# Kernel tuning notes

Hardware: AMD Instinct MI355X
Metric: run time of the kernel (lower is better)

Reference implementation:

```python
import jax, jax.numpy as jnp
import numpy as np

RANK = 16
BN_EPS = 1e-5


def _head(xf, qw, qb, kw, kb, vw, vb, qlw, klw, ow, ob):
    # xf: [B, S, c]  (c = split channels)
    Q = xf @ qw.T + qb
    K = xf @ kw.T + kb
    V = xf @ vw.T + vb
    Ql = Q @ qlw.T                      # [B, S, rank]
    Kl = K @ klw.T                      # [B, S, rank]
    scores = jnp.einsum('bsr,btr->bst', Ql, Kl) / jnp.sqrt(jnp.float32(RANK))
    attn = jax.nn.softmax(scores, axis=-1)   # [B, S, S]
    out = jnp.einsum('bst,btc->bsc', attn, V)
    return out @ ow.T + ob


def _bn(x, g, b):
    # training-mode BatchNorm2d: biased batch stats over (B, H, W)
    m = x.mean(axis=(0, 2, 3), keepdims=True)
    v = x.var(axis=(0, 2, 3), keepdims=True)
    return (x - m) / jnp.sqrt(v + BN_EPS) * g[None, :, None, None] + b[None, :, None, None]


def reference(x, qw, qb, kw, kb, vw, vb, qlw, klw, ow, ob,
              f1w, f1b, f2w, f2b, g1, b1, g2, b2):
    B, C, H, W = x.shape
    sc = C // 4
    S = H * W
    xf = x.reshape(B, C, S).transpose(0, 2, 1)   # [B, S, C]

    outs = []
    prev = jnp.zeros_like(xf[..., :sc])
    for i in range(4):  # hierarchical: head i consumes split_i + out_{i-1}
        xi = xf[..., i * sc:(i + 1) * sc] + prev
        prev = _head(xi, qw[i], qb[i], kw[i], kb[i], vw[i], vb[i],
                     qlw[i], klw[i], ow[i], ob[i])
        outs.append(prev)

    concat = jnp.concatenate(outs, axis=-1).transpose(0, 2, 1).reshape(B, C, H, W)
    out = x + _bn(concat, g1, b1)

    # FFN: 1x1 conv 256->1024, exact GELU, 1x1 conv 1024->256 (dropout = eval / identity)
    h = jnp.einsum('bchw,oc->bohw', out, f1w) + f1b[None, :, None, None]
    h = jax.nn.gelu(h, approximate=False)
    h = jnp.einsum('bchw,oc->bohw', h, f2w) + f2b[None, :, None, None]
    return out + _bn(h, g2, b2)


def setup_inputs() -> dict:
    key = jax.random.key(0)
    ks = jax.random.split(key, 16)
    B, C, H, W = 2, 256, 64, 64
    sc = C // 4
    s = 0.05
    inp = {
        'x':   jax.random.normal(ks[0], (B, C, H, W), jnp.float32),
        'qw':  jax.random.normal(ks[1], (4, sc, sc), jnp.float32) * s,
        'qb':  jnp.zeros((4, sc), jnp.float32),
        'kw':  jax.random.normal(ks[2], (4, sc, sc), jnp.float32) * s,
        'kb':  jnp.zeros((4, sc), jnp.float32),
        'vw':  jax.random.normal(ks[3], (4, sc, sc), jnp.float32) * s,
        'vb':  jnp.zeros((4, sc), jnp.float32),
        'qlw': jax.random.normal(ks[4], (4, RANK, sc), jnp.float32) * s,
        'klw': jax.random.normal(ks[5], (4, RANK, sc), jnp.float32) * s,
        'ow':  jax.random.normal(ks[6], (4, sc, sc), jnp.float32) * s,
        'ob':  jnp.zeros((4, sc), jnp.float32),
        'f1w': jax.random.normal(ks[7], (4 * C, C), jnp.float32) * s,
        'f1b': jnp.zeros((4 * C,), jnp.float32),
        'f2w': jax.random.normal(ks[8], (C, 4 * C), jnp.float32) * s,
        'f2b': jnp.zeros((C,), jnp.float32),
        'g1':  jnp.ones((C,), jnp.float32),
        'b1':  jnp.zeros((C,), jnp.float32),
        'g2':  jnp.ones((C,), jnp.float32),
        'b2':  jnp.zeros((C,), jnp.float32),
    }
    return inp
```

## Files before the change

### kernel.cpp

```cpp
#include <hip/hip_runtime.h>
#include <math.h>

#define SS 4096
#define CC 256
#define NB 2
#define KSPLIT 8
#define KCHUNK (SS / KSPLIT)
#define KT 64
#define QTM 128

typedef __bf16 bf16x8 __attribute__((ext_vector_type(8)));
typedef float f32x4 __attribute__((ext_vector_type(4)));

__device__ inline float b2f(unsigned short u) {
    union { float f; unsigned int i; } x; x.i = ((unsigned int)u) << 16; return x.f;
}

__global__ void prep_weights_kernel(const float* __restrict__ qw, const float* __restrict__ qb,
                                    const float* __restrict__ kw, const float* __restrict__ kb,
                                    const float* __restrict__ qlw, const float* __restrict__ klw,
                                    float* __restrict__ wq, float* __restrict__ wk,
                                    float* __restrict__ bq, float* __restrict__ bk)
{
    int i = blockIdx.x;
    int t = threadIdx.x;
    for (int idx = t; idx < 16 * 64; idx += 256) {
        int r = idx >> 6, c = idx & 63;
        float sq = 0.f, sk = 0.f;
        for (int j = 0; j < 64; ++j) {
            sq += qlw[(i * 16 + r) * 64 + j] * qw[(i * 64 + j) * 64 + c];
            sk += klw[(i * 16 + r) * 64 + j] * kw[(i * 64 + j) * 64 + c];
        }
        wq[i * 1024 + idx] = sq;
        wk[i * 1024 + idx] = sk;
    }
    if (t < 16) {
        float sq = 0.f, sk = 0.f;
        for (int j = 0; j < 64; ++j) {
            sq += qlw[(i * 16 + t) * 64 + j] * qb[i * 64 + j];
            sk += klw[(i * 16 + t) * 64 + j] * kb[i * 64 + j];
        }
        bq[i * 16 + t] = sq;
        bk[i * 16 + t] = sk;
    }
}

__global__ void transpose_x_kernel(const float* __restrict__ x, float* __restrict__ xT)
{
    __shared__ float tile[32][33];
    int b = blockIdx.z;
    int s0 = blockIdx.x * 32, c0 = blockIdx.y * 32;
    int tx = threadIdx.x, ty = threadIdx.y;
    const float* xb = x + (size_t)b * CC * SS;
    for (int j = 0; j < 4; ++j)
        tile[ty + 8 * j][tx] = xb[(size_t)(c0 + ty + 8 * j) * SS + s0 + tx];
    __syncthreads();
    float* xTb = xT + (size_t)b * SS * CC;
    for (int j = 0; j < 4; ++j)
        xTb[(size_t)(s0 + ty + 8 * j) * CC + c0 + tx] = tile[tx][ty + 8 * j];
}

__global__ void f32_to_bf16_kernel(const float* __restrict__ src, __bf16* __restrict__ dst, int n)
{
    int i = (blockIdx.x * 256 + threadIdx.x) * 4;
    if (i < n) {
        float4 v = *(const float4*)&src[i];
        union { uint2 u; __bf16 b[4]; } pk;
        pk.b[0] = (__bf16)v.x; pk.b[1] = (__bf16)v.y;
        pk.b[2] = (__bf16)v.z; pk.b[3] = (__bf16)v.w;
        *(uint2*)&dst[i] = pk.u;
    }
}

__global__ __launch_bounds__(256) void head_qkv_kernel(
    const float* __restrict__ xT, const float* __restrict__ conc,
    const float* __restrict__ wq, const float* __restrict__ wk,
    const float* __restrict__ bq, const float* __restrict__ bk,
    const float* __restrict__ vw, const float* __restrict__ vb,
    __bf16* __restrict__ Qlb, __bf16* __restrict__ Klb, __bf16* __restrict__ Vtb, int head)
{
    __shared__ float swq[16 * 65];
    __shared__ float swk[16 * 65];
    __shared__ float swv[64 * 65];
    __shared__ float sxi[16][65];
    __shared__ float sv16[64][17];
    __shared__ float sbq[16], sbk[16], sbv[64];

    int t = threadIdx.x;
    int b = blockIdx.y;
    int s0 = blockIdx.x * 16;

    for (int idx = t; idx < 16 * 64; idx += 256) {
        int r = idx >> 6, c = idx & 63;
        swq[r * 65 + c] = wq[head * 1024 + idx];
        swk[r * 65 + c] = wk[head * 1024 + idx];
    }
    for (int idx = t; idx < 64 * 64; idx += 256) {
        int r = idx >> 6, c = idx & 63;
        swv[r * 65 + c] = vw[head * 4096 + idx];
    }
    if (t < 16) { sbq[t] = bq[head * 16 + t]; sbk[t] = bk[head * 16 + t]; }
    if (t < 64) sbv[t] = vb[head * 64 + t];

    for (int idx = t; idx < 1024; idx += 256) {
        int r = idx >> 6, c = idx & 63;
        size_t row = (size_t)(b * SS + s0 + r);
        float v = xT[row * CC + head * 64 + c];
        if (head > 0) v += conc[row * CC + (head - 1) * 64 + c];
        sxi[r][c] = v;
    }
    __syncthreads();

    for (int idx = t; idx < 1536; idx += 256) {
        int r = idx / 96, o = idx % 96;
        const float* w;
        float acc;
        int kind;
        if (o < 16)      { w = &swq[o * 65];        acc = sbq[o];      kind = 0; }
        else if (o < 32) { w = &swk[(o - 16) * 65]; acc = sbk[o - 16]; kind = 1; }
        else             { w = &swv[(o - 32) * 65]; acc = sbv[o - 32]; kind = 2; }
        float s = 0.f;
        #pragma unroll 16
        for (int c = 0; c < 64; ++c) s += sxi[r][c] * w[c];
        acc += s;
        size_t row = (size_t)(b * SS + s0 + r);
        if (kind == 0)      Qlb[row * 16 + o] = (__bf16)(acc * 0.25f);
        else if (kind == 1) Klb[row * 16 + (o - 16)] = (__bf16)acc;
        else                sv16[o - 32][r] = acc;
    }
    __syncthreads();

    {
        int c = t >> 2, sq = t & 3;
        union { uint2 u; __bf16 bb[4]; } pk;
        #pragma unroll
        for (int j = 0; j < 4; ++j) pk.bb[j] = (__bf16)sv16[c][sq * 4 + j];
        *(uint2*)&Vtb[((size_t)b * 64 + c) * SS + s0 + sq * 4] = pk.u;
    }
}

__global__ __launch_bounds__(512) void attn_mfma_kernel(
    const __bf16* __restrict__ Qlb, const __bf16* __restrict__ Klb,
    const __bf16* __restrict__ Vtb,
    __bf16* __restrict__ pacc, float* __restrict__ pm, float* __restrict__ pl)
{
    __shared__ __align__(16) __bf16 sK[64 * 24];
    __shared__ __align__(16) __bf16 sVt[64 * 64];
    __shared__ __align__(16) __bf16 sP[8][16 * 64];

    const int t = threadIdx.x;
    const int lane = t & 63, wv = t >> 6;
    const int b = blockIdx.z, chunk = blockIdx.y;
    const int g = lane >> 4, qi = lane & 15;
    const int qrow = blockIdx.x * QTM + wv * 16 + qi;

    bf16x8 bQ;
    #pragma unroll
    for (int j = 0; j < 8; ++j) bQ[j] = (__bf16)0.f;
    if (lane < 32) bQ = *(const bf16x8*)(Qlb + ((size_t)b * SS + qrow) * 16 + g * 8);

    f32x4 acc[4];
    #pragma unroll
    for (int cs = 0; cs < 4; ++cs)
        #pragma unroll
        for (int r = 0; r < 4; ++r) acc[cs][r] = 0.f;
    float mrun = -1e30f, lrun = 0.f;

    __bf16* Pw = &sP[wv][0];
    const size_t kbase = (size_t)b * SS;
    const int kbeg = chunk * KCHUNK;

    for (int kt0 = kbeg; kt0 < kbeg + KCHUNK; kt0 += KT) {
        __syncthreads();
        if (t < 256) {
            int kk = t >> 2, quad = t & 3;
            *(uint2*)((char*)sK + kk * 48 + quad * 8) =
                *(const uint2*)(Klb + (kbase + kt0 + kk) * 16 + quad * 4);
        }
        {
            int c = t >> 3, sl = t & 7;
            int ksrc = (sl ^ (c & 7)) * 8;
            uint4 v = *(const uint4*)(Vtb + ((size_t)b * 64 + c) * SS + kt0 + ksrc);
            *(uint4*)((char*)sVt + c * 128 + sl * 16) = v;
        }
        __syncthreads();

        f32x4 st[4];
        #pragma unroll
        for (int ks = 0; ks < 4; ++ks) {
            bf16x8 aK;
            #pragma unroll
            for (int j = 0; j < 8; ++j) aK[j] = (__bf16)0.f;
            if (lane < 32)
                aK = *(const bf16x8*)((char*)sK + (ks * 16 + qi) * 48 + g * 16);
            f32x4 z;
            #pragma unroll
            for (int r = 0; r < 4; ++r) z[r] = 0.f;
            st[ks] = __builtin_amdgcn_mfma_f32_16x16x32_bf16(aK, bQ, z, 0, 0, 0);
        }

        float tmax = -1e30f;
        #pragma unroll
        for (int ks = 0; ks < 4; ++ks)
            #pragma unroll
            for (int r = 0; r < 4; ++r) tmax = fmaxf(tmax, st[ks][r]);
        tmax = fmaxf(tmax, __shfl_xor(tmax, 16));
        tmax = fmaxf(tmax, __shfl_xor(tmax, 32));
        float mnew = fmaxf(mrun, tmax);
        float scale = __expf(mrun - mnew);
        float psum = 0.f;
        #pragma unroll
        for (int ks = 0; ks < 4; ++ks) {
            union { uint2 u; __bf16 bb[4]; } pk;
            #pragma unroll
            for (int r = 0; r < 4; ++r) {
                float p = __expf(st[ks][r] - mnew);
                psum += p;
                pk.bb[r] = (__bf16)p;
            }
            int off = (qi * 128 + ks * 32 + g * 8) ^ ((qi & 7) << 4);
            *(uint2*)((char*)Pw + off) = pk.u;
        }
        psum += __shfl_xor(psum, 16);
        psum += __shfl_xor(psum, 32);
        lrun = lrun * scale + psum;
        mrun = mnew;
        #pragma unroll
        for (int cs = 0; cs < 4; ++cs) acc[cs] *= scale;

        #pragma unroll
        for (int kc = 0; kc < 2; ++kc) {
            int boff = (qi * 128 + kc * 64 + g * 16) ^ ((qi & 7) << 4);
            bf16x8 bP = *(const bf16x8*)((char*)Pw + boff);
            #pragma unroll
            for (int cs = 0; cs < 4; ++cs) {
                int c = cs * 16 + qi;
                int aoff = (c * 128 + kc * 64 + g * 16) ^ ((c & 7) << 4);
                bf16x8 aV = *(const bf16x8*)((char*)sVt + aoff);
                acc[cs] = __builtin_amdgcn_mfma_f32_16x16x32_bf16(aV, bP, acc[cs], 0, 0, 0);
            }
        }
    }

    size_t prow = (size_t)(b * KSPLIT + chunk) * SS + qrow;
    #pragma unroll
    for (int cs = 0; cs < 4; ++cs) {
        union { uint2 u; __bf16 bb[4]; } pk;
        #pragma unroll
        for (int r = 0; r < 4; ++r) pk.bb[r] = (__bf16)acc[cs][r];
        *(uint2*)(pacc + prow * 64 + cs * 16 + g * 4) = pk.u;
    }
    if (lane < 16) { pm[prow] = mrun; pl[prow] = lrun; }
}

__global__ __launch_bounds__(512) void attn_combine_kernel(
    const __bf16* __restrict__ pacc, const float* __restrict__ pm, const float* __restrict__ pl,
    const float* __restrict__ ow, const float* __restrict__ ob,
    float* __restrict__ conc, int head)
{
    __shared__ float sO[32][66];
    __shared__ float sOWt[64][68];
    __shared__ float sob[64];

    const int t = threadIdx.x;
    const int b = blockIdx.y;
    const int s0 = blockIdx.x * 32;
    const int q = t >> 4;
    const int gk = t & 15;
    const int vc0 = gk * 4;

    for (int idx = t; idx < 4096; idx += 512) {
        int co = idx >> 6, k = idx & 63;
        sOWt[k][co] = ow[head * 4096 + idx];
    }
    if (t < 64) sob[t] = ob[head * 64 + t];

    float pmv[KSPLIT];
    float mstar = -1e30f;
    #pragma unroll
    for (int c = 0; c < KSPLIT; ++c) {
        pmv[c] = pm[(size_t)(b * KSPLIT + c) * SS + s0 + q];
        mstar = fmaxf(mstar, pmv[c]);
    }
    float l = 0.f;
    float o0 = 0.f, o1 = 0.f, o2 = 0.f, o3 = 0.f;
    const unsigned short* pu = (const unsigned short*)pacc;
    #pragma unroll
    for (int c = 0; c < KSPLIT; ++c) {
        size_t prow = (size_t)(b * KSPLIT + c) * SS + s0 + q;
        float w = __expf(pmv[c] - mstar);
        l += w * pl[prow];
        ushort4 a4 = *(const ushort4*)&pu[prow * 64 + vc0];
        o0 += w * b2f(a4.x); o1 += w * b2f(a4.y); o2 += w * b2f(a4.z); o3 += w * b2f(a4.w);
    }
    float inv_l = 1.f / l;
    sO[q][vc0 + 0] = o0 * inv_l;
    sO[q][vc0 + 1] = o1 * inv_l;
    sO[q][vc0 + 2] = o2 * inv_l;
    sO[q][vc0 + 3] = o3 * inv_l;
    __syncthreads();

    float e0 = sob[vc0 + 0], e1 = sob[vc0 + 1], e2 = sob[vc0 + 2], e3 = sob[vc0 + 3];
    #pragma unroll 8
    for (int k = 0; k < 64; ++k) {
        float ov = sO[q][k];
        float4 w4 = *(const float4*)&sOWt[k][vc0];
        e0 += ov * w4.x; e1 += ov * w4.y; e2 += ov * w4.z; e3 += ov * w4.w;
    }
    float* cp = conc + (size_t)(b * SS + s0 + q) * CC + head * 64 + vc0;
    float4 r; r.x = e0; r.y = e1; r.z = e2; r.w = e3;
    *(float4*)cp = r;
}

__global__ void bn_stats_kernel(const float* __restrict__ data, float* __restrict__ sum,
                                float* __restrict__ sumsq, int rows_per_block)
{
    int t = threadIdx.x;
    int r0 = blockIdx.x * rows_per_block;
    float s = 0.f, ss = 0.f;
    for (int r = 0; r < rows_per_block; ++r) {
        float v = data[(size_t)(r0 + r) * CC + t];
        s += v; ss += v * v;
    }
    atomicAdd(&sum[t], s);
    atomicAdd(&sumsq[t], ss);
}

__global__ void bn_apply1_kernel(const float* __restrict__ xT, const float* __restrict__ conc,
                                 const float* __restrict__ sum, const float* __restrict__ sumsq,
                                 const float* __restrict__ g, const float* __restrict__ bta,
                                 float* __restrict__ out1, __bf16* __restrict__ out1b)
{
    size_t idx = (size_t)blockIdx.x * 256 + threadIdx.x;
    int c = threadIdx.x;
    float mean = sum[c] * (1.f / 8192.f);
    float var = sumsq[c] * (1.f / 8192.f) - mean * mean;
    float rstd = rsqrtf(var + 1e-5f);
    float v = xT[idx] + (conc[idx] - mean) * rstd * g[c] + bta[c];
    out1[idx] = v;
    out1b[idx] = (__bf16)v;
}

template<int MREP>
__global__ __launch_bounds__(256) void gemm_mfma_kernel(
    const __bf16* __restrict__ A, const __bf16* __restrict__ W,
    const float* __restrict__ bias, void* __restrict__ out,
    int N, int K, int mode)
{
    constexpr int BM = 2 * MREP * 16;
    __shared__ __align__(16) __bf16 sA[BM * 72];
    __shared__ __align__(16) __bf16 sB[64 * 72];

    const int t = threadIdx.x;
    const int lane = t & 63, wv = t >> 6;
    const int wm = wv & 1, wn = wv >> 1;
    const int g = lane >> 4, c = lane & 15;
    const int m0 = blockIdx.x * BM, n0 = blockIdx.y * 64;

    f32x4 acc[MREP][2];
    #pragma unroll
    for (int mi = 0; mi < MREP; ++mi)
        #pragma unroll
        for (int ni = 0; ni < 2; ++ni)
            #pragma unroll
            for (int r = 0; r < 4; ++r) acc[mi][ni][r] = 0.f;

    const int rS = t >> 3, ksS = (t & 7) * 8;

    for (int k0 = 0; k0 < K; k0 += 64) {
        __syncthreads();
        #pragma unroll
        for (int i = 0; i < MREP; ++i) {
            int r = rS + i * 32;
            *(uint4*)&sA[r * 72 + ksS] = *(const uint4*)&A[(size_t)(m0 + r) * K + k0 + ksS];
        }
        #pragma unroll
        for (int i = 0; i < 2; ++i) {
            int r = rS + i * 32;
            *(uint4*)&sB[r * 72 + ksS] = *(const uint4*)&W[(size_t)(n0 + r) * K + k0 + ksS];
        }
        __syncthreads();

        #pragma unroll
        for (int kk = 0; kk < 2; ++kk) {
            bf16x8 bfr[2];
            #pragma unroll
            for (int ni = 0; ni < 2; ++ni)
                bfr[ni] = *(const bf16x8*)&sB[(wn * 32 + ni * 16 + c) * 72 + kk * 32 + g * 8];
            #pragma unroll
            for (int mi = 0; mi < MREP; ++mi) {
                bf16x8 afr = *(const bf16x8*)&sA[(wm * MREP * 16 + mi * 16 + c) * 72 + kk * 32 + g * 8];
                #pragma unroll
                for (int ni = 0; ni < 2; ++ni)
                    acc[mi][ni] = __builtin_amdgcn_mfma_f32_16x16x32_bf16(afr, bfr[ni], acc[mi][ni], 0, 0, 0);
            }
        }
    }

    #pragma unroll
    for (int ni = 0; ni < 2; ++ni) {
        int col = n0 + wn * 32 + ni * 16 + c;
        float bb = bias[col];
        #pragma unroll
        for (int mi = 0; mi < MREP; ++mi) {
            int row0 = m0 + wm * MREP * 16 + mi * 16 + g * 4;
            #pragma unroll
            for (int r = 0; r < 4; ++r) {
                float v = acc[mi][ni][r] + bb;
                if (mode) {
                    v = 0.5f * v * (1.f + erff(v * 0.70710678118654752f));
                    ((__bf16*)out)[(size_t)(row0 + r) * N + col] = (__bf16)v;
                } else {
                    ((float*)out)[(size_t)(row0 + r) * N + col] = v;
                }
            }
        }
    }
}

__global__ void bn_final_kernel(const float* __restrict__ out1, const float* __restrict__ h2,
                                const float* __restrict__ sum, const float* __restrict__ sumsq,
                                const float* __restrict__ g, const float* __restrict__ bta,
                                float* __restrict__ out)
{
    __shared__ float tile[32][33];
    int b = blockIdx.z;
    int s0 = blockIdx.x * 32, c0 = blockIdx.y * 32;
    int tx = threadIdx.x, ty = threadIdx.y;
    for (int j = 0; j < 4; ++j) {
        int c = c0 + tx;
        int s = s0 + ty + 8 * j;
        size_t idx = ((size_t)b * SS + s) * CC + c;
        float mean = sum[c] * (1.f / 8192.f);
        float var = sumsq[c] * (1.f / 8192.f) - mean * mean;
        float rstd = rsqrtf(var + 1e-5f);
        tile[ty + 8 * j][tx] = out1[idx] + (h2[idx] - mean) * rstd * g[c] + bta[c];
    }
    __syncthreads();
    for (int j = 0; j < 4; ++j) {
        int c = c0 + ty + 8 * j;
        int s = s0 + tx;
        out[((size_t)b * CC + c) * SS + s] = tile[tx][ty + 8 * j];
    }
}

extern "C" void kernel_launch(void* const* d_in, const int* in_sizes, int n_in,
                              void* d_out, int out_size, void* d_ws, size_t ws_size,
                              hipStream_t stream)
{
    const float* x   = (const float*)d_in[0];
    const float* qw  = (const float*)d_in[1];
    const float* qb  = (const float*)d_in[2];
    const float* kw  = (const float*)d_in[3];
    const float* kb  = (const float*)d_in[4];
    const float* vw  = (const float*)d_in[5];
    const float* vb  = (const float*)d_in[6];
    const float* qlw = (const float*)d_in[7];
    const float* klw = (const float*)d_in[8];
    const float* ow  = (const float*)d_in[9];
    const float* ob  = (const float*)d_in[10];
    const float* f1w = (const float*)d_in[11];
    const float* f1b = (const float*)d_in[12];
    const float* f2w = (const float*)d_in[13];
    const float* f2b = (const float*)d_in[14];
    const float* g1  = (const float*)d_in[15];
    const float* b1  = (const float*)d_in[16];
    const float* g2  = (const float*)d_in[17];
    const float* b2  = (const float*)d_in[18];
    float* outp = (float*)d_out;

    float* ws = (float*)d_ws;
    size_t off = 0;
    float* xT    = ws + off; off += (size_t)NB * SS * CC;
    float* conc  = ws + off; off += (size_t)NB * SS * CC;
    float* out1  = ws + off; off += (size_t)NB * SS * CC;
    float* h2    = ws + off; off += (size_t)NB * SS * CC;
    float* Hreg  = ws + off; off += (size_t)NB * SS * 1024 / 2;
    __bf16* out1b = (__bf16*)(ws + off); off += (size_t)NB * SS * CC / 2;
    __bf16* Qlb  = (__bf16*)(ws + off); off += (size_t)NB * SS * 16 / 2;
    __bf16* Klb  = (__bf16*)(ws + off); off += (size_t)NB * SS * 16 / 2;
    __bf16* Vtb  = (__bf16*)(ws + off); off += (size_t)NB * 64 * SS / 2;
    __bf16* f1wb = (__bf16*)(ws + off); off += (size_t)1024 * CC / 2;
    __bf16* f2wb = (__bf16*)(ws + off); off += (size_t)CC * 1024 / 2;
    float* wq_e  = ws + off; off += 4 * 1024;
    float* wk_e  = ws + off; off += 4 * 1024;
    float* bq_e  = ws + off; off += 64;
    float* bk_e  = ws + off; off += 64;
    float* stats = ws + off; off += 1024;
    float* sum1 = stats, *sumsq1 = stats + 256, *sum2 = stats + 512, *sumsq2 = stats + 768;

    __bf16* pacc = (__bf16*)Hreg;
    float* pm = Hreg + (size_t)NB * KSPLIT * SS * 64 / 2;
    float* pl = pm + (size_t)NB * KSPLIT * SS;
    __bf16* h1b = (__bf16*)Hreg;

    hipMemsetAsync(stats, 0, 1024 * sizeof(float), stream);

    prep_weights_kernel<<<4, 256, 0, stream>>>(qw, qb, kw, kb, qlw, klw, wq_e, wk_e, bq_e, bk_e);
    transpose_x_kernel<<<dim3(SS / 32, CC / 32, NB), dim3(32, 8), 0, stream>>>(x, xT);
    f32_to_bf16_kernel<<<(1024 * CC) / 1024, 256, 0, stream>>>(f1w, f1wb, 1024 * CC);
    f32_to_bf16_kernel<<<(CC * 1024) / 1024, 256, 0, stream>>>(f2w, f2wb, CC * 1024);

    for (int head = 0; head < 4; ++head) {
        head_qkv_kernel<<<dim3(SS / 16, NB), 256, 0, stream>>>(
            xT, conc, wq_e, wk_e, bq_e, bk_e, vw, vb, Qlb, Klb, Vtb, head);
        attn_mfma_kernel<<<dim3(SS / QTM, KSPLIT, NB), 512, 0, stream>>>(
            Qlb, Klb, Vtb, pacc, pm, pl);
        attn_combine_kernel<<<dim3(SS / 32, NB), 512, 0, stream>>>(
            pacc, pm, pl, ow, ob, conc, head);
    }

    bn_stats_kernel<<<128, 256, 0, stream>>>(conc, sum1, sumsq1, (NB * SS) / 128);
    bn_apply1_kernel<<<(NB * SS * CC) / 256, 256, 0, stream>>>(
        xT, conc, sum1, sumsq1, g1, b1, out1, out1b);

    gemm_mfma_kernel<4><<<dim3((NB * SS) / 128, 1024 / 64), 256, 0, stream>>>(
        out1b, f1wb, f1b, (void*)h1b, 1024, CC, 1);
    gemm_mfma_kernel<2><<<dim3((NB * SS) / 64, CC / 64), 256, 0, stream>>>(
        h1b, f2wb, f2b, (void*)h2, CC, 1024, 0);

    bn_stats_kernel<<<128, 256, 0, stream>>>(h2, sum2, sumsq2, (NB * SS) / 128);
    bn_final_kernel<<<dim3(SS / 32, CC / 32, NB), dim3(32, 8), 0, stream>>>(
        out1, h2, sum2, sumsq2, g2, b2, outp);
}
```

Before: 362.7 us.

## Use MFMA for head QKV projection, fuse BN stats into producers, store bf16 intermediates

The per-head QKV projection now runs on MFMA with bf16 weights prepacked into one buffer, and each block covers 32 rows instead of 16. BatchNorm statistics are accumulated inside the attention-combine kernel and the second FFN GEMM through shared and global atomics, so both standalone bn_stats passes are gone. The out1 and h2 intermediates are stored only in bf16, which cuts memory traffic but lowers the precision of the residual path and the final output.

```diff
diff --git a/kernel.cpp b/kernel.cpp
--- a/kernel.cpp
+++ b/kernel.cpp
@@ -18,9 +18,9 @@
 
 __global__ void prep_weights_kernel(const float* __restrict__ qw, const float* __restrict__ qb,
                                     const float* __restrict__ kw, const float* __restrict__ kb,
+                                    const float* __restrict__ vw, const float* __restrict__ vb,
                                     const float* __restrict__ qlw, const float* __restrict__ klw,
-                                    float* __restrict__ wq, float* __restrict__ wk,
-                                    float* __restrict__ bq, float* __restrict__ bk)
+                                    __bf16* __restrict__ Wall, float* __restrict__ bias_all)
 {
     int i = blockIdx.x;
     int t = threadIdx.x;
@@ -31,18 +31,21 @@
             sq += qlw[(i * 16 + r) * 64 + j] * qw[(i * 64 + j) * 64 + c];
             sk += klw[(i * 16 + r) * 64 + j] * kw[(i * 64 + j) * 64 + c];
         }
-        wq[i * 1024 + idx] = sq;
-        wk[i * 1024 + idx] = sk;
-    }
+        Wall[i * 6144 + idx] = (__bf16)(0.25f * sq);
+        Wall[i * 6144 + 1024 + idx] = (__bf16)sk;
+    }
+    for (int idx = t; idx < 64 * 64; idx += 256)
+        Wall[i * 6144 + 2048 + idx] = (__bf16)vw[i * 4096 + idx];
     if (t < 16) {
         float sq = 0.f, sk = 0.f;
         for (int j = 0; j < 64; ++j) {
             sq += qlw[(i * 16 + t) * 64 + j] * qb[i * 64 + j];
             sk += klw[(i * 16 + t) * 64 + j] * kb[i * 64 + j];
         }
-        bq[i * 16 + t] = sq;
-        bk[i * 16 + t] = sk;
-    }
+        bias_all[i * 96 + t] = 0.25f * sq;
+        bias_all[i * 96 + 16 + t] = sk;
+    }
+    if (t < 64) bias_all[i * 96 + 32 + t] = vb[i * 64 + t];
 }
 
 __global__ void transpose_x_kernel(const float* __restrict__ x, float* __restrict__ xT)
@@ -72,70 +75,80 @@
     }
 }
 
-__global__ __launch_bounds__(256) void head_qkv_kernel(
+__global__ __launch_bounds__(256) void head_qkv_mfma_kernel(
     const float* __restrict__ xT, const float* __restrict__ conc,
-    const float* __restrict__ wq, const float* __restrict__ wk,
-    const float* __restrict__ bq, const float* __restrict__ bk,
-    const float* __restrict__ vw, const float* __restrict__ vb,
+    const __bf16* __restrict__ Wall, const float* __restrict__ bias_all,
     __bf16* __restrict__ Qlb, __bf16* __restrict__ Klb, __bf16* __restrict__ Vtb, int head)
 {
-    __shared__ float swq[16 * 65];
-    __shared__ float swk[16 * 65];
-    __shared__ float swv[64 * 65];
-    __shared__ float sxi[16][65];
-    __shared__ float sv16[64][17];
-    __shared__ float sbq[16], sbk[16], sbv[64];
-
-    int t = threadIdx.x;
-    int b = blockIdx.y;
-    int s0 = blockIdx.x * 16;
-
-    for (int idx = t; idx < 16 * 64; idx += 256) {
-        int r = idx >> 6, c = idx & 63;
-        swq[r * 65 + c] = wq[head * 1024 + idx];
-        swk[r * 65 + c] = wk[head * 1024 + idx];
-    }
-    for (int idx = t; idx < 64 * 64; idx += 256) {
-        int r = idx >> 6, c = idx & 63;
-        swv[r * 65 + c] = vw[head * 4096 + idx];
-    }
-    if (t < 16) { sbq[t] = bq[head * 16 + t]; sbk[t] = bk[head * 16 + t]; }
-    if (t < 64) sbv[t] = vb[head * 64 + t];
-
-    for (int idx = t; idx < 1024; idx += 256) {
-        int r = idx >> 6, c = idx & 63;
-        size_t row = (size_t)(b * SS + s0 + r);
-        float v = xT[row * CC + head * 64 + c];
-        if (head > 0) v += conc[row * CC + (head - 1) * 64 + c];
-        sxi[r][c] = v;
+    __shared__ __align__(16) __bf16 sXi[32 * 72];
+    __shared__ __align__(16) __bf16 sW[96 * 72];
+    __shared__ __align__(16) __bf16 sVtT[64 * 40];
+    __shared__ float sBias[96];
+
+    const int t = threadIdx.x;
+    const int b = blockIdx.y;
+    const int s0 = blockIdx.x * 32;
+    const int lane = t & 63, wv = t >> 6;
+    const int wm = wv & 1, wnh = wv >> 1;
+    const int c = lane & 15, g = lane >> 4;
+
+    #pragma unroll
+    for (int i = 0; i < 6; ++i) {
+        int e = t + i * 256;
+        int row = e >> 4, c4 = (e & 15) * 4;
+        *(uint2*)&sW[row * 72 + c4] = *(const uint2*)&Wall[head * 6144 + row * 64 + c4];
+    }
+    if (t < 96) sBias[t] = bias_all[head * 96 + t];
+
+    #pragma unroll
+    for (int i = 0; i < 2; ++i) {
+        int idx = t + i * 256;
+        int row = idx >> 4, c4 = (idx & 15) * 4;
+        size_t grow = (size_t)(b * SS + s0 + row);
+        float4 v = *(const float4*)&xT[grow * CC + head * 64 + c4];
+        if (head > 0) {
+            float4 p = *(const float4*)&conc[grow * CC + (head - 1) * 64 + c4];
+            v.x += p.x; v.y += p.y; v.z += p.z; v.w += p.w;
+        }
+        union { uint2 u; __bf16 bb[4]; } pk;
+        pk.bb[0] = (__bf16)v.x; pk.bb[1] = (__bf16)v.y;
+        pk.bb[2] = (__bf16)v.z; pk.bb[3] = (__bf16)v.w;
+        *(uint2*)&sXi[row * 72 + c4] = pk.u;
     }
     __syncthreads();
 
-    for (int idx = t; idx < 1536; idx += 256) {
-        int r = idx / 96, o = idx % 96;
-        const float* w;
-        float acc;
-        int kind;
-        if (o < 16)      { w = &swq[o * 65];        acc = sbq[o];      kind = 0; }
-        else if (o < 32) { w = &swk[(o - 16) * 65]; acc = sbk[o - 16]; kind = 1; }
-        else             { w = &swv[(o - 32) * 65]; acc = sbv[o - 32]; kind = 2; }
-        float s = 0.f;
-        #pragma unroll 16
-        for (int c = 0; c < 64; ++c) s += sxi[r][c] * w[c];
-        acc += s;
-        size_t row = (size_t)(b * SS + s0 + r);
-        if (kind == 0)      Qlb[row * 16 + o] = (__bf16)(acc * 0.25f);
-        else if (kind == 1) Klb[row * 16 + (o - 16)] = (__bf16)acc;
-        else                sv16[o - 32][r] = acc;
+    bf16x8 aX0 = *(const bf16x8*)&sXi[(wm * 16 + c) * 72 + g * 8];
+    bf16x8 aX1 = *(const bf16x8*)&sXi[(wm * 16 + c) * 72 + 32 + g * 8];
+
+    #pragma unroll
+    for (int nt = 0; nt < 3; ++nt) {
+        int ntile = wnh * 3 + nt;
+        bf16x8 bW0 = *(const bf16x8*)&sW[(ntile * 16 + c) * 72 + g * 8];
+        bf16x8 bW1 = *(const bf16x8*)&sW[(ntile * 16 + c) * 72 + 32 + g * 8];
+        f32x4 d;
+        #pragma unroll
+        for (int r = 0; r < 4; ++r) d[r] = 0.f;
+        d = __builtin_amdgcn_mfma_f32_16x16x32_bf16(aX0, bW0, d, 0, 0, 0);
+        d = __builtin_amdgcn_mfma_f32_16x16x32_bf16(aX1, bW1, d, 0, 0, 0);
+
+        int ch = ntile * 16 + c;
+        float bb = sBias[ch];
+        int srow_l0 = wm * 16 + g * 4;
+        #pragma unroll
+        for (int r = 0; r < 4; ++r) {
+            float v = d[r] + bb;
+            int srow = s0 + srow_l0 + r;
+            if (ntile == 0)      Qlb[((size_t)b * SS + srow) * 16 + ch] = (__bf16)v;
+            else if (ntile == 1) Klb[((size_t)b * SS + srow) * 16 + (ch - 16)] = (__bf16)v;
+            else                 sVtT[(ch - 32) * 40 + srow_l0 + r] = (__bf16)v;
+        }
     }
     __syncthreads();
 
     {
-        int c = t >> 2, sq = t & 3;
-        union { uint2 u; __bf16 bb[4]; } pk;
-        #pragma unroll
-        for (int j = 0; j < 4; ++j) pk.bb[j] = (__bf16)sv16[c][sq * 4 + j];
-        *(uint2*)&Vtb[((size_t)b * 64 + c) * SS + s0 + sq * 4] = pk.u;
+        int ch = t >> 2, chunk = t & 3;
+        *(uint4*)&Vtb[((size_t)b * 64 + ch) * SS + s0 + chunk * 8] =
+            *(const uint4*)&sVtT[ch * 40 + chunk * 8];
     }
 }
 
@@ -256,11 +269,12 @@
 __global__ __launch_bounds__(512) void attn_combine_kernel(
     const __bf16* __restrict__ pacc, const float* __restrict__ pm, const float* __restrict__ pl,
     const float* __restrict__ ow, const float* __restrict__ ob,
-    float* __restrict__ conc, int head)
+    float* __restrict__ conc, float* __restrict__ gsum, float* __restrict__ gss, int head)
 {
     __shared__ float sO[32][66];
     __shared__ float sOWt[64][68];
     __shared__ float sob[64];
+    __shared__ float lsum[64], lss[64];
 
     const int t = threadIdx.x;
     const int b = blockIdx.y;
@@ -269,6 +283,7 @@
     const int gk = t & 15;
     const int vc0 = gk * 4;
 
+    if (t < 64) { lsum[t] = 0.f; lss[t] = 0.f; }
     for (int idx = t; idx < 4096; idx += 512) {
         int co = idx >> 6, k = idx & 63;
         sOWt[k][co] = ow[head * 4096 + idx];
@@ -300,36 +315,45 @@
     sO[q][vc0 + 3] = o3 * inv_l;
     __syncthreads();
 
-    float e0 = sob[vc0 + 0], e1 = sob[vc0 + 1], e2 = sob[vc0 + 2], e3 = sob[vc0 + 3];
+    float e[4];
+    #pragma unroll
+    for (int j = 0; j < 4; ++j) e[j] = sob[vc0 + j];
     #pragma unroll 8
     for (int k = 0; k < 64; ++k) {
         float ov = sO[q][k];
         float4 w4 = *(const float4*)&sOWt[k][vc0];
-        e0 += ov * w4.x; e1 += ov * w4.y; e2 += ov * w4.z; e3 += ov * w4.w;
+        e[0] += ov * w4.x; e[1] += ov * w4.y; e[2] += ov * w4.z; e[3] += ov * w4.w;
     }
     float* cp = conc + (size_t)(b * SS + s0 + q) * CC + head * 64 + vc0;
-    float4 r; r.x = e0; r.y = e1; r.z = e2; r.w = e3;
+    float4 r; r.x = e[0]; r.y = e[1]; r.z = e[2]; r.w = e[3];
     *(float4*)cp = r;
-}
-
-__global__ void bn_stats_kernel(const float* __restrict__ data, float* __restrict__ sum,
-                                float* __restrict__ sumsq, int rows_per_block)
-{
-    int t = threadIdx.x;
-    int r0 = blockIdx.x * rows_per_block;
-    float s = 0.f, ss = 0.f;
-    for (int r = 0; r < rows_per_block; ++r) {
-        float v = data[(size_t)(r0 + r) * CC + t];
-        s += v; ss += v * v;
-    }
-    atomicAdd(&sum[t], s);
-    atomicAdd(&sumsq[t], ss);
+
+    float sv[4], sq[4];
+    #pragma unroll
+    for (int j = 0; j < 4; ++j) { sv[j] = e[j]; sq[j] = e[j] * e[j]; }
+    #pragma unroll
+    for (int j = 0; j < 4; ++j) {
+        sv[j] += __shfl_xor(sv[j], 16); sv[j] += __shfl_xor(sv[j], 32);
+        sq[j] += __shfl_xor(sq[j], 16); sq[j] += __shfl_xor(sq[j], 32);
+    }
+    if ((t & 48) == 0) {
+        #pragma unroll
+        for (int j = 0; j < 4; ++j) {
+            atomicAdd(&lsum[vc0 + j], sv[j]);
+            atomicAdd(&lss[vc0 + j], sq[j]);
+        }
+    }
+    __syncthreads();
+    if (t < 64) {
+        atomicAdd(&gsum[head * 64 + t], lsum[t]);
+        atomicAdd(&gss[head * 64 + t], lss[t]);
+    }
 }
 
 __global__ void bn_apply1_kernel(const float* __restrict__ xT, const float* __restrict__ conc,
                                  const float* __restrict__ sum, const float* __restrict__ sumsq,
                                  const float* __restrict__ g, const float* __restrict__ bta,
-                                 float* __restrict__ out1, __bf16* __restrict__ out1b)
+                                 __bf16* __restrict__ out1b)
 {
     size_t idx = (size_t)blockIdx.x * 256 + threadIdx.x;
     int c = threadIdx.x;
@@ -337,16 +361,14 @@
     float var = sumsq[c] * (1.f / 8192.f) - mean * mean;
     float rstd = rsqrtf(var + 1e-5f);
     float v = xT[idx] + (conc[idx] - mean) * rstd * g[c] + bta[c];
-    out1[idx] = v;
     out1b[idx] = (__bf16)v;
 }
 
-template<int MREP>
-__global__ __launch_bounds__(256) void gemm_mfma_kernel(
+__global__ __launch_bounds__(256) void gemm1_mfma_kernel(
     const __bf16* __restrict__ A, const __bf16* __restrict__ W,
-    const float* __restrict__ bias, void* __restrict__ out,
-    int N, int K, int mode)
-{
+    const float* __restrict__ bias, __bf16* __restrict__ out, int N, int K)
+{
+    constexpr int MREP = 4;
     constexpr int BM = 2 * MREP * 16;
     __shared__ __align__(16) __bf16 sA[BM * 72];
     __shared__ __align__(16) __bf16 sB[64 * 72];
@@ -407,18 +429,102 @@
             #pragma unroll
             for (int r = 0; r < 4; ++r) {
                 float v = acc[mi][ni][r] + bb;
-                if (mode) {
-                    v = 0.5f * v * (1.f + erff(v * 0.70710678118654752f));
-                    ((__bf16*)out)[(size_t)(row0 + r) * N + col] = (__bf16)v;
-                } else {
-                    ((float*)out)[(size_t)(row0 + r) * N + col] = v;
-                }
+                v = 0.5f * v * (1.f + erff(v * 0.70710678118654752f));
+                out[(size_t)(row0 + r) * N + col] = (__bf16)v;
             }
         }
     }
 }
 
-__global__ void bn_final_kernel(const float* __restrict__ out1, const float* __restrict__ h2,
+__global__ __launch_bounds__(256) void gemm2_mfma_stats_kernel(
+    const __bf16* __restrict__ A, const __bf16* __restrict__ W,
+    const float* __restrict__ bias, __bf16* __restrict__ out,
+    float* __restrict__ gsum, float* __restrict__ gss, int N, int K)
+{
+    constexpr int MREP = 2;
+    constexpr int BM = 2 * MREP * 16;
+    __shared__ __align__(16) __bf16 sA[BM * 72];
+    __shared__ __align__(16) __bf16 sB[64 * 72];
+    __shared__ float lsum[64], lss[64];
+
+    const int t = threadIdx.x;
+    const int lane = t & 63, wv = t >> 6;
+    const int wm = wv & 1, wn = wv >> 1;
+    const int g = lane >> 4, c = lane & 15;
+    const int m0 = blockIdx.x * BM, n0 = blockIdx.y * 64;
+
+    if (t < 64) { lsum[t] = 0.f; lss[t] = 0.f; }
+
+    f32x4 acc[MREP][2];
+    #pragma unroll
+    for (int mi = 0; mi < MREP; ++mi)
+        #pragma unroll
+        for (int ni = 0; ni < 2; ++ni)
+            #pragma unroll
+            for (int r = 0; r < 4; ++r) acc[mi][ni][r] = 0.f;
+
+    const int rS = t >> 3, ksS = (t & 7) * 8;
+
+    for (int k0 = 0; k0 < K; k0 += 64) {
+        __syncthreads();
+        #pragma unroll
+        for (int i = 0; i < MREP; ++i) {
+            int r = rS + i * 32;
+            *(uint4*)&sA[r * 72 + ksS] = *(const uint4*)&A[(size_t)(m0 + r) * K + k0 + ksS];
+        }
+        #pragma unroll
+        for (int i = 0; i < 2; ++i) {
+            int r = rS + i * 32;
+            *(uint4*)&sB[r * 72 + ksS] = *(const uint4*)&W[(size_t)(n0 + r) * K + k0 + ksS];
+        }
+        __syncthreads();
+
+        #pragma unroll
+        for (int kk = 0; kk < 2; ++kk) {
+            bf16x8 bfr[2];
+            #pragma unroll
+            for (int ni = 0; ni < 2; ++ni)
+                bfr[ni] = *(const bf16x8*)&sB[(wn * 32 + ni * 16 + c) * 72 + kk * 32 + g * 8];
+            #pragma unroll
+            for (int mi = 0; mi < MREP; ++mi) {
+                bf16x8 afr = *(const bf16x8*)&sA[(wm * MREP * 16 + mi * 16 + c) * 72 + kk * 32 + g * 8];
+                #pragma unroll
+                for (int ni = 0; ni < 2; ++ni)
+                    acc[mi][ni] = __builtin_amdgcn_mfma_f32_16x16x32_bf16(afr, bfr[ni], acc[mi][ni], 0, 0, 0);
+            }
+        }
+    }
+
+    #pragma unroll
+    for (int ni = 0; ni < 2; ++ni) {
+        int col = n0 + wn * 32 + ni * 16 + c;
+        float bb = bias[col];
+        float ps = 0.f, pss = 0.f;
+        #pragma unroll
+        for (int mi = 0; mi < MREP; ++mi) {
+            int row0 = m0 + wm * MREP * 16 + mi * 16 + g * 4;
+            #pragma unroll
+            for (int r = 0; r < 4; ++r) {
+                float v = acc[mi][ni][r] + bb;
+                out[(size_t)(row0 + r) * N + col] = (__bf16)v;
+                ps += v; pss += v * v;
+            }
+        }
+        ps += __shfl_xor(ps, 16); ps += __shfl_xor(ps, 32);
+        pss += __shfl_xor(pss, 16); pss += __shfl_xor(pss, 32);
+        if ((t & 48) == 0) {
+            atomicAdd(&lsum[wn * 32 + ni * 16 + c], ps);
+            atomicAdd(&lss[wn * 32 + ni * 16 + c], pss);
+        }
+    }
+    __syncthreads();
+    if (t < 64) {
+        atomicAdd(&gsum[n0 + t], lsum[t]);
+        atomicAdd(&gss[n0 + t], lss[t]);
+    }
+}
+
+__global__ void bn_final_kernel(const __bf16* __restrict__ out1b, const __bf16* __restrict__ h2b,
                                 const float* __restrict__ sum, const float* __restrict__ sumsq,
                                 const float* __restrict__ g, const float* __restrict__ bta,
                                 float* __restrict__ out)
@@ -427,6 +533,8 @@
     int b = blockIdx.z;
     int s0 = blockIdx.x * 32, c0 = blockIdx.y * 32;
     int tx = threadIdx.x, ty = threadIdx.y;
+    const unsigned short* o1 = (const unsigned short*)out1b;
+    const unsigned short* h2 = (const unsigned short*)h2b;
     for (int j = 0; j < 4; ++j) {
         int c = c0 + tx;
         int s = s0 + ty + 8 * j;
@@ -434,7 +542,7 @@
         float mean = sum[c] * (1.f / 8192.f);
         float var = sumsq[c] * (1.f / 8192.f) - mean * mean;
         float rstd = rsqrtf(var + 1e-5f);
-        tile[ty + 8 * j][tx] = out1[idx] + (h2[idx] - mean) * rstd * g[c] + bta[c];
+        tile[ty + 8 * j][tx] = b2f(o1[idx]) + (b2f(h2[idx]) - mean) * rstd * g[c] + bta[c];
     }
     __syncthreads();
     for (int j = 0; j < 4; ++j) {
@@ -473,19 +581,16 @@
     size_t off = 0;
     float* xT    = ws + off; off += (size_t)NB * SS * CC;
     float* conc  = ws + off; off += (size_t)NB * SS * CC;
-    float* out1  = ws + off; off += (size_t)NB * SS * CC;
-    float* h2    = ws + off; off += (size_t)NB * SS * CC;
     float* Hreg  = ws + off; off += (size_t)NB * SS * 1024 / 2;
     __bf16* out1b = (__bf16*)(ws + off); off += (size_t)NB * SS * CC / 2;
+    __bf16* h2b   = (__bf16*)(ws + off); off += (size_t)NB * SS * CC / 2;
     __bf16* Qlb  = (__bf16*)(ws + off); off += (size_t)NB * SS * 16 / 2;
     __bf16* Klb  = (__bf16*)(ws + off); off += (size_t)NB * SS * 16 / 2;
     __bf16* Vtb  = (__bf16*)(ws + off); off += (size_t)NB * 64 * SS / 2;
     __bf16* f1wb = (__bf16*)(ws + off); off += (size_t)1024 * CC / 2;
     __bf16* f2wb = (__bf16*)(ws + off); off += (size_t)CC * 1024 / 2;
-    float* wq_e  = ws + off; off += 4 * 1024;
-    float* wk_e  = ws + off; off += 4 * 1024;
-    float* bq_e  = ws + off; off += 64;
-    float* bk_e  = ws + off; off += 64;
+    __bf16* Wall = (__bf16*)(ws + off); off += 4 * 6144 / 2;
+    float* bias_all = ws + off; off += 4 * 96;
     float* stats = ws + off; off += 1024;
     float* sum1 = stats, *sumsq1 = stats + 256, *sum2 = stats + 512, *sumsq2 = stats + 768;
 
@@ -496,30 +601,28 @@
 
     hipMemsetAsync(stats, 0, 1024 * sizeof(float), stream);
 
-    prep_weights_kernel<<<4, 256, 0, stream>>>(qw, qb, kw, kb, qlw, klw, wq_e, wk_e, bq_e, bk_e);
+    prep_weights_kernel<<<4, 256, 0, stream>>>(qw, qb, kw, kb, vw, vb, qlw, klw, Wall, bias_all);
     transpose_x_kernel<<<dim3(SS / 32, CC / 32, NB), dim3(32, 8), 0, stream>>>(x, xT);
     f32_to_bf16_kernel<<<(1024 * CC) / 1024, 256, 0, stream>>>(f1w, f1wb, 1024 * CC);
     f32_to_bf16_kernel<<<(CC * 1024) / 1024, 256, 0, stream>>>(f2w, f2wb, CC * 1024);
 
     for (int head = 0; head < 4; ++head) {
-        head_qkv_kernel<<<dim3(SS / 16, NB), 256, 0, stream>>>(
-            xT, conc, wq_e, wk_e, bq_e, bk_e, vw, vb, Qlb, Klb, Vtb, head);
+        head_qkv_mfma_kernel<<<dim3(SS / 32, NB), 256, 0, stream>>>(
+            xT, conc, Wall, bias_all, Qlb, Klb, Vtb, head);
         attn_mfma_kernel<<<dim3(SS / QTM, KSPLIT, NB), 512, 0, stream>>>(
             Qlb, Klb, Vtb, pacc, pm, pl);
         attn_combine_kernel<<<dim3(SS / 32, NB), 512, 0, stream>>>(
-            pacc, pm, pl, ow, ob, conc, head);
-    }
-
-    bn_stats_kernel<<<128, 256, 0, stream>>>(conc, sum1, sumsq1, (NB * SS) / 128);
+            pacc, pm, pl, ow, ob, conc, sum1, sumsq1, head);
+    }
+
     bn_apply1_kernel<<<(NB * SS * CC) / 256, 256, 0, stream>>>(
-        xT, conc, sum1, sumsq1, g1, b1, out1, out1b);
-
-    gemm_mfma_kernel<4><<<dim3((NB * SS) / 128, 1024 / 64), 256, 0, stream>>>(
-        out1b, f1wb, f1b, (void*)h1b, 1024, CC, 1);
-    gemm_mfma_kernel<2><<<dim3((NB * SS) / 64, CC / 64), 256, 0, stream>>>(
-        h1b, f2wb, f2b, (void*)h2, CC, 1024, 0);
-
-    bn_stats_kernel<<<128, 256, 0, stream>>>(h2, sum2, sumsq2, (NB * SS) / 128);
+        xT, conc, sum1, sumsq1, g1, b1, out1b);
+
+    gemm1_mfma_kernel<<<dim3((NB * SS) / 128, 1024 / 64), 256, 0, stream>>>(
+        out1b, f1wb, f1b, h1b, 1024, CC);
+    gemm2_mfma_stats_kernel<<<dim3((NB * SS) / 64, CC / 64), 256, 0, stream>>>(
+        h1b, f2wb, f2b, h2b, sum2, sumsq2, CC, 1024);
+
     bn_final_kernel<<<dim3(SS / 32, CC / 32, NB), dim3(32, 8), 0, stream>>>(
-        out1, h2, sum2, sumsq2, g2, b2, outp);
-}
+        out1b, h2b, sum2, sumsq2, g2, b2, outp);
+}
```

Result: faster. 322.7 us (-11.0%).
